# Kernel optimization log

Measured on AMD Instinct MI355X. Metric: run time of the kernel, lower is better.

## Reference

```python
import jax, jax.numpy as jnp
import numpy as np

B, T, HID = 2, 2048, 2048
NH, NKV, HD = 32, 8, 64


def setup_inputs() -> dict:
    key = jax.random.key(0)
    ks = jax.random.split(key, 5)
    x = jax.random.normal(ks[0], (B, T, HID), dtype=jnp.float32)
    position_ids = jnp.broadcast_to(jnp.arange(T, dtype=jnp.int32), (B, T))
    s = 0.02
    Wq = jax.random.normal(ks[1], (NH * HD, HID), dtype=jnp.float32) * s
    Wk = jax.random.normal(ks[2], (NKV * HD, HID), dtype=jnp.float32) * s
    Wv = jax.random.normal(ks[3], (NKV * HD, HID), dtype=jnp.float32) * s
    Wo = jax.random.normal(ks[4], (HID, NH * HD), dtype=jnp.float32) * s
    return {"x": x, "position_ids": position_ids, "Wq": Wq, "Wk": Wk, "Wv": Wv, "Wo": Wo}


def _rotate_half(t):
    t1, t2 = jnp.split(t, 2, axis=-1)
    return jnp.concatenate([-t2, t1], axis=-1)


def reference(x, position_ids, Wq, Wk, Wv, Wo):
    Bd, Td, _ = x.shape
    q = (x @ Wq.T).reshape(Bd, Td, NH, HD)
    k = (x @ Wk.T).reshape(Bd, Td, NKV, HD)
    v = (x @ Wv.T).reshape(Bd, Td, NKV, HD)

    # DummyRotaryEmbedding: freqs over even indices, repeat_interleave(2)
    freqs = 1.0 / (10000.0 ** (jnp.arange(0, HD, 2, dtype=jnp.float32) / HD))
    angles = position_ids.astype(jnp.float32)[:, :, None] * freqs  # [B,T,HD/2]
    cos = jnp.repeat(jnp.cos(angles), 2, axis=-1)[:, :, None, :]   # [B,T,1,HD]
    sin = jnp.repeat(jnp.sin(angles), 2, axis=-1)[:, :, None, :]

    q = q * cos + _rotate_half(q) * sin
    k = k * cos + _rotate_half(k) * sin

    n_rep = NH // NKV
    k = jnp.repeat(k, n_rep, axis=2)  # [B,T,NH,HD]
    v = jnp.repeat(v, n_rep, axis=2)

    scale = 1.0 / np.sqrt(HD).astype(np.float32)
    scores = jnp.einsum('bqhd,bkhd->bhqk', q, k) * scale  # [B,NH,T,T]
    probs = jax.nn.softmax(scores, axis=-1)
    out = jnp.einsum('bhqk,bkhd->bqhd', probs, v).reshape(Bd, Td, NH * HD)
    return out @ Wo.T
```

## Files before the change

### kernel.cpp

```cpp
#include <hip/hip_runtime.h>
#include <hip/hip_bf16.h>
#include <stdint.h>


typedef __attribute__((ext_vector_type(8))) short short8;
typedef __attribute__((ext_vector_type(4))) float f32x4;
typedef __attribute__((ext_vector_type(16))) float f32x16;

__device__ __forceinline__ unsigned short f2bf(float f) {
  union { float f; uint32_t u; } x; x.f = f;
  uint32_t r = x.u + 0x7fffu + ((x.u >> 16) & 1u);
  return (unsigned short)(r >> 16);
}
__device__ __forceinline__ float bf2f(unsigned short u) {
  union { uint32_t u; float f; } x; x.u = ((uint32_t)u) << 16;
  return x.f;
}
__device__ __forceinline__ uint32_t cvt_pk_bf16(float a, float b) {
  uint32_t r;
  asm("v_cvt_pk_bf16_f32 %0, %1, %2" : "=v"(r) : "v"(a), "v"(b));
  return r;
}
__device__ __forceinline__ void pl32swap(uint32_t& dst, uint32_t& src) {
  asm("v_permlane32_swap_b32 %0, %1" : "+v"(dst), "+v"(src));
}

__device__ __forceinline__ void gload_lds16(const void* g, void* l) {
  __builtin_amdgcn_global_load_lds(
      (const __attribute__((address_space(1))) unsigned int*)g,
      (__attribute__((address_space(3))) unsigned int*)l, 16, 0, 0);
}

#define VMCNT(n) asm volatile("s_waitcnt vmcnt(" #n ")" ::: "memory")
#define LGKMCNT0 asm volatile("s_waitcnt lgkmcnt(0)" ::: "memory")

__global__ __launch_bounds__(256) void convert_kernel(
    const float* __restrict__ x, const float* __restrict__ Wq,
    const float* __restrict__ Wk, const float* __restrict__ Wv,
    const float* __restrict__ Wo,
    unsigned short* __restrict__ xb, unsigned short* __restrict__ wqkvb,
    unsigned short* __restrict__ wob) {
  const int NX = 2097152;
  const int NQ = 1048576;
  const int NK = 262144;
  const int NV = 262144;
  const int NO = 1048576;
  const int total = NX + NQ + NK + NV + NO;
  for (int i = blockIdx.x * blockDim.x + threadIdx.x; i < total;
       i += gridDim.x * blockDim.x) {
    const float4* s; unsigned short* d; int o;
    if (i < NX)                 { o = i;               s = (const float4*)x;  d = xb; }
    else if (i < NX+NQ)         { o = i-NX;            s = (const float4*)Wq; d = wqkvb; }
    else if (i < NX+NQ+NK)      { o = i-NX-NQ;         s = (const float4*)Wk; d = wqkvb + 4194304; }
    else if (i < NX+NQ+NK+NV)   { o = i-NX-NQ-NK;      s = (const float4*)Wv; d = wqkvb + 5242880; }
    else                        { o = i-NX-NQ-NK-NV;   s = (const float4*)Wo; d = wob; }
    float4 v = s[o];
    ushort4 r;
    r.x = f2bf(v.x); r.y = f2bf(v.y); r.z = f2bf(v.z); r.w = f2bf(v.w);
    *(ushort4*)(d + (size_t)o * 4) = r;
  }
}

template <int NQ, typename OutT>
__global__ __launch_bounds__(512, 1) void gemm_8p(
    const unsigned short* __restrict__ A, const unsigned short* __restrict__ Bt,
    OutT* __restrict__ C, int N, int K) {
  __shared__ unsigned short lA[2][256 * 64];
  __shared__ unsigned short lB[2][NQ * 64 * 64];
  const int tid  = threadIdx.x;
  const int lane = tid & 63;
  const int w    = tid >> 6;
  const int wr   = w >> 2, wc = w & 3;
  const long tm  = (long)blockIdx.y * 256;
  const long tn  = (long)blockIdx.x * (NQ * 64);

  f32x4 acc[2][4][NQ];
#pragma unroll
  for (int mq = 0; mq < 2; ++mq)
#pragma unroll
    for (int fi = 0; fi < 4; ++fi)
#pragma unroll
      for (int nq = 0; nq < NQ; ++nq) acc[mq][fi][nq] = (f32x4){0.f, 0.f, 0.f, 0.f};

  const int srow = tid >> 3;
  const int sgr  = ((tid & 7) ^ (srow & 7)) * 8;
  const unsigned short* ga = A  + (tm + srow) * (long)K + sgr;
  const unsigned short* gb = Bt + (tn + srow) * (long)K + sgr;

  int aoff[2][4][2], boff[NQ][2];
#pragma unroll
  for (int mq = 0; mq < 2; ++mq)
#pragma unroll
    for (int fi = 0; fi < 4; ++fi)
#pragma unroll
      for (int ks = 0; ks < 2; ++ks) {
        int gk = (lane >> 4) + ks * 4;
        aoff[mq][fi][ks] = (wr * 128 + mq * 64 + fi * 16 + (lane & 15)) * 128 +
                           ((gk ^ (lane & 7)) << 4);
      }
#pragma unroll
  for (int nq = 0; nq < NQ; ++nq)
#pragma unroll
    for (int ks = 0; ks < 2; ++ks) {
      int gk = (lane >> 4) + ks * 4;
      boff[nq][ks] = (wc * (NQ * 16) + nq * 16 + (lane & 15)) * 128 +
                     ((gk ^ (lane & 7)) << 4);
    }

#pragma unroll
  for (int i = 0; i < 4; ++i)  gload_lds16(ga + (long)(64 * i) * K, &lA[0][tid * 8 + 4096 * i]);
#pragma unroll
  for (int i = 0; i < NQ; ++i) gload_lds16(gb + (long)(64 * i) * K, &lB[0][tid * 8 + 4096 * i]);
  VMCNT(0);
  __builtin_amdgcn_s_barrier();

  const int nk = K >> 6;
  for (int t = 0; t < nk; ++t) {
    const int slot = t & 1;
    const unsigned short* gaT = ga + (long)((t + 1) << 6);
    const unsigned short* gbT = gb + (long)((t + 1) << 6);
    const bool st = (t + 1 < nk);
    const char* As = (const char*)lA[slot];
    const char* Bs = (const char*)lB[slot];
    unsigned short* dA = &lA[slot ^ 1][tid * 8];
    unsigned short* dB = &lB[slot ^ 1][tid * 8];

    short8 bf[NQ][2];
#pragma unroll
    for (int mq = 0; mq < 2; ++mq) {
      short8 af[4][2];
#pragma unroll
      for (int nq = 0; nq < NQ; ++nq) {
        if (nq == 0) {
#pragma unroll
          for (int fi = 0; fi < 4; ++fi)
#pragma unroll
            for (int ks = 0; ks < 2; ++ks)
              af[fi][ks] = *(const short8*)(As + aoff[mq][fi][ks]);
        }
        if (mq == 0) {
#pragma unroll
          for (int ks = 0; ks < 2; ++ks)
            bf[nq][ks] = *(const short8*)(Bs + boff[nq][ks]);
        }
        if (st) {
          const int p = mq * NQ + nq;
          if (p == 0) {
            gload_lds16(gaT,                  dA);
            gload_lds16(gaT + (long)64 * K,   dA + 4096);
          } else if (p == 1) {
            gload_lds16(gaT + (long)128 * K,  dA + 8192);
            gload_lds16(gaT + (long)192 * K,  dA + 12288);
          } else if (p == 2) {
#pragma unroll
            for (int i = 0; i < NQ; ++i)
              gload_lds16(gbT + (long)(64 * i) * K, dB + 4096 * i);
          }
        }
        __builtin_amdgcn_s_barrier();
        LGKMCNT0;
        __builtin_amdgcn_sched_barrier(0);
        __builtin_amdgcn_s_setprio(1);
#pragma unroll
        for (int ks = 0; ks < 2; ++ks)
#pragma unroll
          for (int fi = 0; fi < 4; ++fi)
            acc[mq][fi][nq] = __builtin_amdgcn_mfma_f32_16x16x32_bf16(
                af[fi][ks], bf[nq][ks], acc[mq][fi][nq], 0, 0, 0);
        __builtin_amdgcn_s_setprio(0);
        __builtin_amdgcn_sched_barrier(0);
        if (mq == 1 && nq == NQ - 1) VMCNT(0);
        __builtin_amdgcn_s_barrier();
      }
    }
  }

#pragma unroll
  for (int mq = 0; mq < 2; ++mq)
#pragma unroll
    for (int fi = 0; fi < 4; ++fi)
#pragma unroll
      for (int nq = 0; nq < NQ; ++nq) {
        long col = tn + wc * (NQ * 16) + nq * 16 + (lane & 15);
#pragma unroll
        for (int i = 0; i < 4; ++i) {
          long row = tm + wr * 128 + mq * 64 + fi * 16 + (lane >> 4) * 4 + i;
          float v = acc[mq][fi][nq][i];
          if constexpr (sizeof(OutT) == 2) C[row * N + col] = (OutT)f2bf(v);
          else                             C[row * N + col] = (OutT)v;
        }
      }
}

__global__ __launch_bounds__(256) void rope_kernel(
    unsigned short* __restrict__ qkv, const int* __restrict__ pos_ids,
    unsigned short* __restrict__ Vt) {
  const int m = blockIdx.x;
  const int b = m >> 11, t = m & 2047;
  const int tid = threadIdx.x;
  const float QSCALE = 0.18033688011112042f;
  __shared__ float cs[32], sn[32];
  if (tid < 32) {
    float pos = (float)pos_ids[m];
    float a = pos * exp2f(-(float)tid * 0.4152410118609203f);
    float s_, c_;
    sincosf(a, &s_, &c_);
    cs[tid] = c_; sn[tid] = s_;
  }
  __syncthreads();
  unsigned short* row = qkv + (size_t)m * 3072;

  const int qc = tid * 8;
  short8 qa = *(const short8*)(row + qc);
  short8 qp = *(const short8*)(row + (qc ^ 32));
  short8 ka = {}, kp = {};
  if (tid < 64) {
    const int kc = 2048 + tid * 8;
    ka = *(const short8*)(row + kc);
    kp = *(const short8*)(row + (kc ^ 32));
  }
  __syncthreads();

  {
    const int dbase = qc & 63;
    const float sgn = (qc & 32) ? 1.0f : -1.0f;
    short8 out;
#pragma unroll
    for (int j = 0; j < 8; ++j) {
      int fi = (dbase + j) >> 1;
      float o = bf2f((unsigned short)qa[j]) * cs[fi] +
                sgn * bf2f((unsigned short)qp[j]) * sn[fi];
      out[j] = (short)f2bf(o * QSCALE);
    }
    *(short8*)(row + qc) = out;
  }
  if (tid < 64) {
    const int kc = 2048 + tid * 8;
    const int dbase = (tid * 8) & 63;
    const float sgn = ((tid * 8) & 32) ? 1.0f : -1.0f;
    short8 out;
#pragma unroll
    for (int j = 0; j < 8; ++j) {
      int fi = (dbase + j) >> 1;
      float o = bf2f((unsigned short)ka[j]) * cs[fi] +
                sgn * bf2f((unsigned short)kp[j]) * sn[fi];
      out[j] = (short)f2bf(o);
    }
    *(short8*)(row + kc) = out;
  }
  {
    int e = tid * 2;
    unsigned short v0 = row[2560 + e];
    unsigned short v1 = row[2560 + e + 1];
    int g = e >> 6, d = e & 63;
    unsigned short* vt = Vt + ((size_t)((b * 8 + g) * 64 + d)) * 2048 + t;
    vt[0] = v0;
    vt[2048] = v1;
  }
}

__global__ __launch_bounds__(512) void attn_kernel(
    const unsigned short* __restrict__ qkv,
    const unsigned short* __restrict__ Vt,
    unsigned short* __restrict__ attnout) {
  const int qt = blockIdx.x, g = blockIdx.y, b = blockIdx.z;
  const int tid = threadIdx.x, lane = tid & 63, w = tid >> 6;
  const int l31 = lane & 31, hi = lane >> 5;
  const int h = g * 4 + (w & 3);
  const int qbase = qt * 64 + (w >> 2) * 32;

  __shared__ unsigned short lK[2][64 * 64];
  __shared__ unsigned short lV[3][64 * 64];

  short8 qf[4];
  {
    const unsigned short* qrow =
        qkv + ((size_t)(b * 2048 + qbase + l31)) * 3072 + h * 64 + hi * 8;
#pragma unroll
    for (int kc = 0; kc < 4; ++kc) qf[kc] = *(const short8*)(qrow + kc * 16);
  }

  f32x16 o0, o1;
#pragma unroll
  for (int i = 0; i < 16; ++i) { o0[i] = 0.f; o1[i] = 0.f; }
  float lrun = 0.f;

  const unsigned short* kgbase = qkv + (size_t)b * 2048 * 3072 + 2048 + g * 64;
  const unsigned short* vgbase = Vt + ((size_t)(b * 8 + g) * 64) * 2048;
  const int srow = w * 8 + (lane >> 3);
  const int sg = ((lane & 7) ^ (srow & 7)) * 8;

  int koff[2][4];
#pragma unroll
  for (int s = 0; s < 2; ++s)
#pragma unroll
    for (int kc = 0; kc < 4; ++kc) {
      int r = s * 32 + l31;
      koff[s][kc] = r * 128 + (((kc * 2 + hi) ^ (r & 7)) << 4);
    }

#define STAGE(kbuf, vbuf, kb)                                                       \
  {                                                                                 \
    const unsigned short* kk_ = kgbase + (size_t)((kb) * 64) * 3072;                \
    const unsigned short* vv_ = vgbase + (kb) * 64;                                 \
    gload_lds16(kk_ + (size_t)srow * 3072 + sg, &lK[kbuf][(w * 8) * 64]);           \
    gload_lds16(vv_ + (size_t)srow * 2048 + sg, &lV[vbuf][(w * 8) * 64]);           \
  }

#define PV_BLOCK(VBASE)                                                             \
  {                                                                                 \
    const char* Vb_ = (VBASE);                                                      \
    _Pragma("unroll")                                                               \
    for (int ks = 0; ks < 2; ++ks) {                                                \
      union { uint32_t u[4]; short8 s8; } fa, fb;                                   \
      _Pragma("unroll")                                                             \
      for (int u = 0; u < 4; ++u) { fa.u[u] = wd[ks][u]; fb.u[u] = wd[ks][4 + u]; } \
      const int kk0 = ks * 2, kk1 = ks * 2 + 1;                                     \
      short8 va0 = *(const short8*)(Vb_ + koff[0][kk0]);                            \
      short8 va1 = *(const short8*)(Vb_ + koff[1][kk0]);                            \
      o0 = __builtin_amdgcn_mfma_f32_32x32x16_bf16(fa.s8, va0, o0, 0, 0, 0);        \
      o1 = __builtin_amdgcn_mfma_f32_32x32x16_bf16(fa.s8, va1, o1, 0, 0, 0);        \
      short8 vb0 = *(const short8*)(Vb_ + koff[0][kk1]);                            \
      short8 vb1 = *(const short8*)(Vb_ + koff[1][kk1]);                            \
      o0 = __builtin_amdgcn_mfma_f32_32x32x16_bf16(fb.s8, vb0, o0, 0, 0, 0);        \
      o1 = __builtin_amdgcn_mfma_f32_32x32x16_bf16(fb.s8, vb1, o1, 0, 0, 0);        \
    }                                                                               \
  }

  uint32_t wd[2][8];

  STAGE(0, 0, 0);
  __syncthreads();

  int vnext = 1;
#pragma unroll 1
  for (int t = 0; t < 32; ++t) {
    if (t + 1 < 32) STAGE((t + 1) & 1, vnext, t + 1);
    const char* Kb = (const char*)lK[t & 1];
    const int vprev = (vnext == 2) ? 0 : vnext + 1;

    f32x16 s0, s1;
#pragma unroll
    for (int i = 0; i < 16; ++i) { s0[i] = 0.f; s1[i] = 0.f; }
    __builtin_amdgcn_s_setprio(1);
#pragma unroll
    for (int kc = 0; kc < 4; ++kc) {
      short8 k0 = *(const short8*)(Kb + koff[0][kc]);
      short8 k1 = *(const short8*)(Kb + koff[1][kc]);
      s0 = __builtin_amdgcn_mfma_f32_32x32x16_bf16(k0, qf[kc], s0, 0, 0, 0);
      s1 = __builtin_amdgcn_mfma_f32_32x32x16_bf16(k1, qf[kc], s1, 0, 0, 0);
    }
    if (t > 0) PV_BLOCK((const char*)lV[vprev]);
    __builtin_amdgcn_s_setprio(0);

    float rs = 0.f;
#pragma unroll
    for (int i = 0; i < 16; ++i) { s0[i] = __builtin_amdgcn_exp2f(s0[i]); rs += s0[i]; }
#pragma unroll
    for (int i = 0; i < 16; ++i) { s1[i] = __builtin_amdgcn_exp2f(s1[i]); rs += s1[i]; }
    rs += __shfl_xor(rs, 32);
    lrun += rs;

#pragma unroll
    for (int mi = 0; mi < 8; ++mi) {
      wd[0][mi] = cvt_pk_bf16(s0[2 * mi], s0[2 * mi + 1]);
      wd[1][mi] = cvt_pk_bf16(s1[2 * mi], s1[2 * mi + 1]);
    }
#pragma unroll
    for (int ks = 0; ks < 2; ++ks) {
      pl32swap(wd[ks][0], wd[ks][2]);
      pl32swap(wd[ks][1], wd[ks][3]);
      pl32swap(wd[ks][4], wd[ks][6]);
      pl32swap(wd[ks][5], wd[ks][7]);
    }

    vnext = (vnext == 2) ? 0 : vnext + 1;
    __syncthreads();
  }

  PV_BLOCK((const char*)lV[1]);

  float inv = 1.0f / lrun;
  const size_t obase =
      (size_t)(b * 2048 + qbase) * 2048 + h * 64 + l31;
#pragma unroll
  for (int reg = 0; reg < 16; ++reg) {
    int q = (reg & 3) + 8 * (reg >> 2) + 4 * hi;
    float invq = __shfl(inv, q);
    attnout[obase + (size_t)q * 2048]      = f2bf(o0[reg] * invq);
    attnout[obase + (size_t)q * 2048 + 32] = f2bf(o1[reg] * invq);
  }
#undef STAGE
#undef PV_BLOCK
}

extern "C" void kernel_launch(void* const* d_in, const int* in_sizes, int n_in,
                              void* d_out, int out_size, void* d_ws, size_t ws_size,
                              hipStream_t stream) {
  (void)in_sizes; (void)n_in; (void)out_size; (void)ws_size;
  const float* x  = (const float*)d_in[0];
  const int* pos  = (const int*)d_in[1];
  const float* Wq = (const float*)d_in[2];
  const float* Wk = (const float*)d_in[3];
  const float* Wv = (const float*)d_in[4];
  const float* Wo = (const float*)d_in[5];
  float* out = (float*)d_out;
  char* ws = (char*)d_ws;

  unsigned short* xb      = (unsigned short*)(ws);
  unsigned short* wqkvb   = (unsigned short*)(ws + 16777216);
  unsigned short* wob     = (unsigned short*)(ws + 29360128);
  unsigned short* qkv     = (unsigned short*)(ws + 37748736);
  unsigned short* Vt      = (unsigned short*)(ws + 62914560);
  unsigned short* attnout = (unsigned short*)(ws + 67108864);

  convert_kernel<<<2048, 256, 0, stream>>>(x, Wq, Wk, Wv, Wo, xb, wqkvb, wob);
  gemm_8p<3, unsigned short><<<dim3(16, 16), 512, 0, stream>>>(xb, wqkvb, qkv, 3072, 2048);
  rope_kernel<<<4096, 256, 0, stream>>>(qkv, pos, Vt);
  attn_kernel<<<dim3(32, 8, 2), 512, 0, stream>>>(qkv, Vt, attnout);
  gemm_8p<2, float><<<dim3(16, 16), 512, 0, stream>>>(attnout, wob, out, 2048, 2048);
}
```

Measured before the change: 214.7 us.

## Halve GEMM M-tile to 128 rows for two blocks per CU; defer softmax row-sum shuffle

Measured after the change: 202.0 us. 5.9% less time.

```diff
diff --git a/kernel.cpp b/kernel.cpp
--- a/kernel.cpp
+++ b/kernel.cpp
@@ -62,53 +62,47 @@
 }
 
 template <int NQ, typename OutT>
-__global__ __launch_bounds__(512, 1) void gemm_8p(
+__global__ __launch_bounds__(512, 2) void gemm_2cu(
     const unsigned short* __restrict__ A, const unsigned short* __restrict__ Bt,
     OutT* __restrict__ C, int N, int K) {
-  __shared__ unsigned short lA[2][256 * 64];
+  __shared__ unsigned short lA[2][128 * 64];
   __shared__ unsigned short lB[2][NQ * 64 * 64];
   const int tid  = threadIdx.x;
   const int lane = tid & 63;
   const int w    = tid >> 6;
   const int wr   = w >> 2, wc = w & 3;
-  const long tm  = (long)blockIdx.y * 256;
+  const long tm  = (long)blockIdx.y * 128;
   const long tn  = (long)blockIdx.x * (NQ * 64);
 
-  f32x4 acc[2][4][NQ];
-#pragma unroll
-  for (int mq = 0; mq < 2; ++mq)
-#pragma unroll
-    for (int fi = 0; fi < 4; ++fi)
-#pragma unroll
-      for (int nq = 0; nq < NQ; ++nq) acc[mq][fi][nq] = (f32x4){0.f, 0.f, 0.f, 0.f};
+  f32x4 acc[4][NQ];
+#pragma unroll
+  for (int fi = 0; fi < 4; ++fi)
+#pragma unroll
+    for (int nq = 0; nq < NQ; ++nq) acc[fi][nq] = (f32x4){0.f, 0.f, 0.f, 0.f};
 
   const int srow = tid >> 3;
   const int sgr  = ((tid & 7) ^ (srow & 7)) * 8;
   const unsigned short* ga = A  + (tm + srow) * (long)K + sgr;
   const unsigned short* gb = Bt + (tn + srow) * (long)K + sgr;
 
-  int aoff[2][4][2], boff[NQ][2];
-#pragma unroll
-  for (int mq = 0; mq < 2; ++mq)
-#pragma unroll
-    for (int fi = 0; fi < 4; ++fi)
-#pragma unroll
-      for (int ks = 0; ks < 2; ++ks) {
-        int gk = (lane >> 4) + ks * 4;
-        aoff[mq][fi][ks] = (wr * 128 + mq * 64 + fi * 16 + (lane & 15)) * 128 +
-                           ((gk ^ (lane & 7)) << 4);
-      }
-#pragma unroll
-  for (int nq = 0; nq < NQ; ++nq)
+  int aoff[4][2], boff[NQ][2];
+#pragma unroll
+  for (int fi = 0; fi < 4; ++fi)
 #pragma unroll
     for (int ks = 0; ks < 2; ++ks) {
       int gk = (lane >> 4) + ks * 4;
-      boff[nq][ks] = (wc * (NQ * 16) + nq * 16 + (lane & 15)) * 128 +
-                     ((gk ^ (lane & 7)) << 4);
-    }
-
-#pragma unroll
-  for (int i = 0; i < 4; ++i)  gload_lds16(ga + (long)(64 * i) * K, &lA[0][tid * 8 + 4096 * i]);
+      aoff[fi][ks] = (wr * 64 + fi * 16 + (lane & 15)) * 128 + ((gk ^ (lane & 7)) << 4);
+    }
+#pragma unroll
+  for (int nq = 0; nq < NQ; ++nq)
+#pragma unroll
+    for (int ks = 0; ks < 2; ++ks) {
+      int gk = (lane >> 4) + ks * 4;
+      boff[nq][ks] = (wc * (NQ * 16) + nq * 16 + (lane & 15)) * 128 + ((gk ^ (lane & 7)) << 4);
+    }
+
+#pragma unroll
+  for (int i = 0; i < 2; ++i)  gload_lds16(ga + (long)(64 * i) * K, &lA[0][tid * 8 + 4096 * i]);
 #pragma unroll
   for (int i = 0; i < NQ; ++i) gload_lds16(gb + (long)(64 * i) * K, &lB[0][tid * 8 + 4096 * i]);
   VMCNT(0);
@@ -125,71 +119,55 @@
     unsigned short* dA = &lA[slot ^ 1][tid * 8];
     unsigned short* dB = &lB[slot ^ 1][tid * 8];
 
-    short8 bf[NQ][2];
-#pragma unroll
-    for (int mq = 0; mq < 2; ++mq) {
-      short8 af[4][2];
-#pragma unroll
-      for (int nq = 0; nq < NQ; ++nq) {
-        if (nq == 0) {
-#pragma unroll
-          for (int fi = 0; fi < 4; ++fi)
-#pragma unroll
-            for (int ks = 0; ks < 2; ++ks)
-              af[fi][ks] = *(const short8*)(As + aoff[mq][fi][ks]);
-        }
-        if (mq == 0) {
+    short8 af[4][2];
+#pragma unroll
+    for (int nq = 0; nq < NQ; ++nq) {
+      if (nq == 0) {
+#pragma unroll
+        for (int fi = 0; fi < 4; ++fi)
 #pragma unroll
           for (int ks = 0; ks < 2; ++ks)
-            bf[nq][ks] = *(const short8*)(Bs + boff[nq][ks]);
-        }
-        if (st) {
-          const int p = mq * NQ + nq;
-          if (p == 0) {
-            gload_lds16(gaT,                  dA);
-            gload_lds16(gaT + (long)64 * K,   dA + 4096);
-          } else if (p == 1) {
-            gload_lds16(gaT + (long)128 * K,  dA + 8192);
-            gload_lds16(gaT + (long)192 * K,  dA + 12288);
-          } else if (p == 2) {
-#pragma unroll
-            for (int i = 0; i < NQ; ++i)
-              gload_lds16(gbT + (long)(64 * i) * K, dB + 4096 * i);
-          }
-        }
-        __builtin_amdgcn_s_barrier();
-        LGKMCNT0;
-        __builtin_amdgcn_sched_barrier(0);
-        __builtin_amdgcn_s_setprio(1);
-#pragma unroll
-        for (int ks = 0; ks < 2; ++ks)
-#pragma unroll
-          for (int fi = 0; fi < 4; ++fi)
-            acc[mq][fi][nq] = __builtin_amdgcn_mfma_f32_16x16x32_bf16(
-                af[fi][ks], bf[nq][ks], acc[mq][fi][nq], 0, 0, 0);
-        __builtin_amdgcn_s_setprio(0);
-        __builtin_amdgcn_sched_barrier(0);
-        if (mq == 1 && nq == NQ - 1) VMCNT(0);
-        __builtin_amdgcn_s_barrier();
+            af[fi][ks] = *(const short8*)(As + aoff[fi][ks]);
       }
-    }
-  }
-
-#pragma unroll
-  for (int mq = 0; mq < 2; ++mq)
-#pragma unroll
-    for (int fi = 0; fi < 4; ++fi)
-#pragma unroll
-      for (int nq = 0; nq < NQ; ++nq) {
-        long col = tn + wc * (NQ * 16) + nq * 16 + (lane & 15);
-#pragma unroll
-        for (int i = 0; i < 4; ++i) {
-          long row = tm + wr * 128 + mq * 64 + fi * 16 + (lane >> 4) * 4 + i;
-          float v = acc[mq][fi][nq][i];
-          if constexpr (sizeof(OutT) == 2) C[row * N + col] = (OutT)f2bf(v);
-          else                             C[row * N + col] = (OutT)v;
-        }
+      short8 bf0 = *(const short8*)(Bs + boff[nq][0]);
+      short8 bf1 = *(const short8*)(Bs + boff[nq][1]);
+      if (st && nq == 0) {
+        gload_lds16(gaT,                 dA);
+        gload_lds16(gaT + (long)64 * K,  dA + 4096);
+#pragma unroll
+        for (int i = 0; i < NQ; ++i)
+          gload_lds16(gbT + (long)(64 * i) * K, dB + 4096 * i);
       }
+      __builtin_amdgcn_s_barrier();
+      LGKMCNT0;
+      __builtin_amdgcn_sched_barrier(0);
+      __builtin_amdgcn_s_setprio(1);
+#pragma unroll
+      for (int fi = 0; fi < 4; ++fi)
+        acc[fi][nq] = __builtin_amdgcn_mfma_f32_16x16x32_bf16(af[fi][0], bf0, acc[fi][nq], 0, 0, 0);
+#pragma unroll
+      for (int fi = 0; fi < 4; ++fi)
+        acc[fi][nq] = __builtin_amdgcn_mfma_f32_16x16x32_bf16(af[fi][1], bf1, acc[fi][nq], 0, 0, 0);
+      __builtin_amdgcn_s_setprio(0);
+      __builtin_amdgcn_sched_barrier(0);
+      if (nq == NQ - 1) VMCNT(0);
+      __builtin_amdgcn_s_barrier();
+    }
+  }
+
+#pragma unroll
+  for (int fi = 0; fi < 4; ++fi)
+#pragma unroll
+    for (int nq = 0; nq < NQ; ++nq) {
+      long col = tn + wc * (NQ * 16) + nq * 16 + (lane & 15);
+#pragma unroll
+      for (int i = 0; i < 4; ++i) {
+        long row = tm + wr * 64 + fi * 16 + (lane >> 4) * 4 + i;
+        float v = acc[fi][nq][i];
+        if constexpr (sizeof(OutT) == 2) C[row * N + col] = (OutT)f2bf(v);
+        else                             C[row * N + col] = (OutT)v;
+      }
+    }
 }
 
 __global__ __launch_bounds__(256) void rope_kernel(
@@ -353,13 +331,10 @@
     if (t > 0) PV_BLOCK((const char*)lV[vprev]);
     __builtin_amdgcn_s_setprio(0);
 
-    float rs = 0.f;
-#pragma unroll
-    for (int i = 0; i < 16; ++i) { s0[i] = __builtin_amdgcn_exp2f(s0[i]); rs += s0[i]; }
-#pragma unroll
-    for (int i = 0; i < 16; ++i) { s1[i] = __builtin_amdgcn_exp2f(s1[i]); rs += s1[i]; }
-    rs += __shfl_xor(rs, 32);
-    lrun += rs;
+#pragma unroll
+    for (int i = 0; i < 16; ++i) { s0[i] = __builtin_amdgcn_exp2f(s0[i]); lrun += s0[i]; }
+#pragma unroll
+    for (int i = 0; i < 16; ++i) { s1[i] = __builtin_amdgcn_exp2f(s1[i]); lrun += s1[i]; }
 
 #pragma unroll
     for (int mi = 0; mi < 8; ++mi) {
@@ -380,6 +355,7 @@
 
   PV_BLOCK((const char*)lV[1]);
 
+  lrun += __shfl_xor(lrun, 32);
   float inv = 1.0f / lrun;
   const size_t obase =
       (size_t)(b * 2048 + qbase) * 2048 + h * 64 + l31;
@@ -415,8 +391,8 @@
   unsigned short* attnout = (unsigned short*)(ws + 67108864);
 
   convert_kernel<<<2048, 256, 0, stream>>>(x, Wq, Wk, Wv, Wo, xb, wqkvb, wob);
-  gemm_8p<3, unsigned short><<<dim3(16, 16), 512, 0, stream>>>(xb, wqkvb, qkv, 3072, 2048);
+  gemm_2cu<3, unsigned short><<<dim3(16, 32), 512, 0, stream>>>(xb, wqkvb, qkv, 3072, 2048);
   rope_kernel<<<4096, 256, 0, stream>>>(qkv, pos, Vt);
   attn_kernel<<<dim3(32, 8, 2), 512, 0, stream>>>(qkv, Vt, attnout);
-  gemm_8p<2, float><<<dim3(16, 16), 512, 0, stream>>>(attnout, wob, out, 2048, 2048);
-}
+  gemm_2cu<2, float><<<dim3(16, 32), 512, 0, stream>>>(attnout, wob, out, 2048, 2048);
+}
```
